# Optimization experiments

Hardware: AMD Instinct MI355X
Metric: run time of the kernel (lower is better)

The kernel has to match this reference:

```python
import jax, jax.numpy as jnp
import numpy as np

N_NODES = 100000
N_EDGES = 1600000
D = 128
NUM_CLASSES = 2
NEG_SLOPE = 0.01  # torch default leaky_relu slope


def setup_inputs() -> dict:
    key = jax.random.key(0)
    ks = jax.random.split(key, 12)
    s = 1.0 / np.sqrt(2 * D)
    return {
        "x": jax.random.normal(ks[0], (N_NODES, D), dtype=jnp.float32),
        "edge_src": jax.random.randint(ks[1], (N_EDGES,), 0, N_NODES, dtype=jnp.int32),
        "edge_dst": jax.random.randint(ks[2], (N_EDGES,), 0, N_NODES, dtype=jnp.int32),
        "edge_w1": jax.random.uniform(ks[3], (N_EDGES,), dtype=jnp.float32),
        "edge_w2": jax.random.uniform(ks[4], (N_EDGES,), dtype=jnp.float32),
        "W1": jax.random.normal(ks[5], (2 * D, D), dtype=jnp.float32) * s,
        "b1": jnp.zeros((D,), dtype=jnp.float32),
        "W2": jax.random.normal(ks[6], (2 * D, D), dtype=jnp.float32) * s,
        "b2": jnp.zeros((D,), dtype=jnp.float32),
        "Wl1": jax.random.normal(ks[7], (D, D), dtype=jnp.float32) * (1.0 / np.sqrt(D)),
        "bl1": jnp.zeros((D,), dtype=jnp.float32),
        "Wl2": jax.random.normal(ks[8], (D, NUM_CLASSES), dtype=jnp.float32) * (1.0 / np.sqrt(D)),
        "bl2": jnp.zeros((NUM_CLASSES,), dtype=jnp.float32),
    }


def _sage_conv(x, src, dst, ew, W, b, deg_inv):
    # weighted SpMM with reduce='mean': sum_e(w_e * x[src_e]) / rowcount(dst)
    msg = ew[:, None] * x[src]                                   # [E, D]
    agg = jax.ops.segment_sum(msg, dst, num_segments=N_NODES)    # [N, D]
    agg = agg * deg_inv[:, None]
    agg = jax.nn.leaky_relu(agg, NEG_SLOPE)
    h = jnp.concatenate([x, agg], axis=-1)                       # [N, 2D]
    return h @ W + b


def reference(x, edge_src, edge_dst, edge_w1, edge_w2,
              W1, b1, W2, b2, Wl1, bl1, Wl2, bl2):
    deg = jax.ops.segment_sum(jnp.ones((N_EDGES,), jnp.float32), edge_dst,
                              num_segments=N_NODES)
    deg_inv = jnp.where(deg > 0, 1.0 / jnp.maximum(deg, 1.0), 0.0)
    h = jax.nn.relu(_sage_conv(x, edge_src, edge_dst, edge_w1, W1, b1, deg_inv))
    h = jax.nn.relu(_sage_conv(h, edge_src, edge_dst, edge_w2, W2, b2, deg_inv))
    # train_status=False -> dropout is identity
    scores = jax.nn.relu(h @ Wl1 + bl1)
    scores = scores @ Wl2 + bl2                                  # [N, num_classes]
    return scores
```

## Files before the change

kernel.cpp:

```cpp
#include <hip/hip_runtime.h>
#include <hip/hip_fp16.h>

#define N_NODES 100000
#define N_EDGES 1600000
#define D 128

#define NBIN 196
#define NCHUNK 391
#define CHUNK_E 4096
#define SCAN_TOT (NBIN * NCHUNK)
#define SC_NB ((SCAN_TOT + 1023) / 1024)

#define WT_BLK 320
#define CVT_BLK 6250

typedef __attribute__((ext_vector_type(8))) _Float16 f16x8;
typedef __attribute__((ext_vector_type(4))) float f32x4;

__device__ __forceinline__ float h2f(ushort u) {
    __half_raw r; r.x = u;
    return __half2float(__half(r));
}
__device__ __forceinline__ ushort f2h(float f) {
    __half_raw r = __half_raw(__float2half(f));
    return r.x;
}


__global__ __launch_bounds__(256) void prep_kernel(const int* __restrict__ dst,
                                                   int* __restrict__ blockhist,
                                                   const float* __restrict__ W1,
                                                   const float* __restrict__ W2,
                                                   const float* __restrict__ Wl1,
                                                   ushort* __restrict__ W1t,
                                                   ushort* __restrict__ W2t,
                                                   ushort* __restrict__ Wl1t,
                                                   const float* __restrict__ x,
                                                   ushort* __restrict__ xf) {
    __shared__ int h[NBIN];
    int tid = threadIdx.x;
    int b = blockIdx.x;
    if (b < NCHUNK) {
        for (int i = tid; i < NBIN; i += 256) h[i] = 0;
        __syncthreads();
        int base = b * CHUNK_E;
#pragma unroll
        for (int j = 0; j < 16; ++j) {
            int i = base + j * 256 + tid;
            if (i < N_EDGES) atomicAdd(&h[dst[i] >> 9], 1);
        }
        __syncthreads();
        for (int i = tid; i < NBIN; i += 256)
            blockhist[i * NCHUNK + b] = h[i];
    } else if (b < NCHUNK + WT_BLK) {
        int i = (b - NCHUNK) * 256 + tid;
        const int DD2 = 2 * D * D;
        const float* src; ushort* dstp; int j;
        if (i < DD2)                  { src = W1;  dstp = W1t;  j = i; }
        else if (i < 2 * DD2)         { src = W2;  dstp = W2t;  j = i - DD2; }
        else                          { src = Wl1; dstp = Wl1t; j = i - 2 * DD2; }
        int k = j >> 7, n = j & 127;
        int addr = (((k >> 3) << 7) + n) * 8 + (k & 7);
        dstp[addr] = f2h(src[j]);
    } else {
        long i = ((long)(b - NCHUNK - WT_BLK) * 256 + tid) * 8;
        const float4 a = *reinterpret_cast<const float4*>(&x[i]);
        const float4 c = *reinterpret_cast<const float4*>(&x[i + 4]);
        ushort4 u0, u1;
        u0.x = f2h(a.x); u0.y = f2h(a.y); u0.z = f2h(a.z); u0.w = f2h(a.w);
        u1.x = f2h(c.x); u1.y = f2h(c.y); u1.z = f2h(c.z); u1.w = f2h(c.w);
        *reinterpret_cast<ushort4*>(&xf[i]) = u0;
        *reinterpret_cast<ushort4*>(&xf[i + 4]) = u1;
    }
}


__global__ __launch_bounds__(256) void scan_a(const int* __restrict__ bh,
                                              int* __restrict__ partials) {
    __shared__ int sums[256];
    int tid = threadIdx.x;
    int base = blockIdx.x * 1024 + tid * 4;
    int s = 0;
#pragma unroll
    for (int i = 0; i < 4; ++i) {
        int idx = base + i;
        if (idx < SCAN_TOT) s += bh[idx];
    }
    sums[tid] = s;
    __syncthreads();
#pragma unroll
    for (int off = 128; off > 0; off >>= 1) {
        if (tid < off) sums[tid] += sums[tid + off];
        __syncthreads();
    }
    if (tid == 0) partials[blockIdx.x] = sums[0];
}

__global__ __launch_bounds__(256) void scan_c(int* __restrict__ bh,
                                              const int* __restrict__ partials,
                                              int* __restrict__ row_ptr) {
    __shared__ int tsum[256];
    __shared__ int red[128];
    __shared__ int offs;
    int tid = threadIdx.x;

    if (tid < 128) {
        int v = (tid < blockIdx.x) ? partials[tid] : 0;
        red[tid] = v;
    }
    __syncthreads();
#pragma unroll
    for (int off = 64; off > 0; off >>= 1) {
        if (tid < off) red[tid] += red[tid + off];
        __syncthreads();
    }
    if (tid == 0) {
        offs = red[0];
        if (blockIdx.x == 0) row_ptr[N_NODES] = N_EDGES;
    }
    __syncthreads();

    int base = blockIdx.x * 1024 + tid * 4;
    int d[4];
#pragma unroll
    for (int i = 0; i < 4; ++i)
        d[i] = (base + i < SCAN_TOT) ? bh[base + i] : 0;
    int s = d[0] + d[1] + d[2] + d[3];
    tsum[tid] = s;
    __syncthreads();
    for (int off = 1; off < 256; off <<= 1) {
        int t = (tid >= off) ? tsum[tid - off] : 0;
        __syncthreads();
        tsum[tid] += t;
        __syncthreads();
    }
    int run = offs + tsum[tid] - s;
#pragma unroll
    for (int i = 0; i < 4; ++i) {
        int idx = base + i;
        if (idx < SCAN_TOT) {
            bh[idx] = run;
            run += d[i];
        }
    }
}

__global__ __launch_bounds__(256) void p1_scatter(const int* __restrict__ src,
                                                  const int* __restrict__ dst,
                                                  const float* __restrict__ w1,
                                                  const float* __restrict__ w2,
                                                  const int* __restrict__ bh,
                                                  uint2* __restrict__ part) {
    __shared__ int cur[NBIN];
    int tid = threadIdx.x;
    for (int b = tid; b < NBIN; b += 256) cur[b] = bh[b * NCHUNK + blockIdx.x];
    __syncthreads();
    int base = blockIdx.x * CHUNK_E;
#pragma unroll
    for (int j = 0; j < 16; ++j) {
        int i = base + j * 256 + tid;
        if (i < N_EDGES) {
            int d = dst[i];
            int pos = atomicAdd(&cur[d >> 9], 1);
            uint2 e;
            e.x = (unsigned)src[i] | ((unsigned)(d & 511) << 17);
            e.y = (unsigned)f2h(w1[i]) | ((unsigned)f2h(w2[i]) << 16);
            part[pos] = e;
        }
    }
}


__global__ __launch_bounds__(256) void p2_kernel(const int* __restrict__ bh,
                                                 const uint2* __restrict__ part,
                                                 int* __restrict__ row_ptr,
                                                 uint2* __restrict__ packed) {
    __shared__ int deg2[512];
    __shared__ int cur[512];
    __shared__ int sb[256];
    int tid = threadIdx.x;
    int bin = blockIdx.x;
    int base = bh[bin * NCHUNK];
    int endv = (bin == NBIN - 1) ? N_EDGES : bh[(bin + 1) * NCHUNK];
    int cnt = endv - base;
    deg2[tid] = 0; deg2[tid + 256] = 0;
    __syncthreads();
    for (int k = tid; k < cnt; k += 256)
        atomicAdd(&deg2[part[base + k].x >> 17], 1);
    __syncthreads();
    int s0 = deg2[2 * tid], s1 = deg2[2 * tid + 1];
    int ts = s0 + s1;
    sb[tid] = ts;
    __syncthreads();
    for (int off = 1; off < 256; off <<= 1) {
        int v = (tid >= off) ? sb[tid - off] : 0;
        __syncthreads();
        sb[tid] += v;
        __syncthreads();
    }
    int ex = sb[tid] - ts;
    cur[2 * tid] = ex;
    cur[2 * tid + 1] = ex + s0;
    int node0 = bin * 512 + 2 * tid;
    if (node0 < N_NODES)     row_ptr[node0]     = base + ex;
    if (node0 + 1 < N_NODES) row_ptr[node0 + 1] = base + ex + s0;
    __syncthreads();
    for (int k = tid; k < cnt; k += 256) {
        uint2 r = part[base + k];
        int local = r.x >> 17;
        float di = 1.0f / (float)deg2[local];
        int pos = base + atomicAdd(&cur[local], 1);
        uint2 e;
        e.x = r.x & 0x1FFFFu;
        e.y = (unsigned)f2h(h2f((ushort)(r.y & 0xFFFFu)) * di)
            | ((unsigned)f2h(h2f((ushort)(r.y >> 16)) * di) << 16);
        packed[pos] = e;
    }
}


template<int WIDX>
__global__ __launch_bounds__(256) void spmm_kernel(const ushort* __restrict__ xin,
                                                   const uint2* __restrict__ edges,
                                                   const int* __restrict__ row_ptr,
                                                   ushort* __restrict__ out) {
    int wid = threadIdx.x >> 6;
    int lane = threadIdx.x & 63;
    int par = lane >> 4;
    int dl = lane & 15;
    int n = blockIdx.x * 4 + wid;
    int beg = row_ptr[n], end = row_ptr[n + 1];
    float a[8] = {0.f, 0.f, 0.f, 0.f, 0.f, 0.f, 0.f, 0.f};

    const _Float16* xh = reinterpret_cast<const _Float16*>(xin);

    int i = beg;
    for (; i + 15 < end; i += 16) {
        const uint2 e0 = edges[i + par];
        const uint2 e1 = edges[i + 4 + par];
        const uint2 e2 = edges[i + 8 + par];
        const uint2 e3 = edges[i + 12 + par];
        float w0 = (float)__builtin_bit_cast(_Float16, (ushort)(WIDX ? (e0.y >> 16) : (e0.y & 0xFFFFu)));
        float w1 = (float)__builtin_bit_cast(_Float16, (ushort)(WIDX ? (e1.y >> 16) : (e1.y & 0xFFFFu)));
        float w2 = (float)__builtin_bit_cast(_Float16, (ushort)(WIDX ? (e2.y >> 16) : (e2.y & 0xFFFFu)));
        float w3 = (float)__builtin_bit_cast(_Float16, (ushort)(WIDX ? (e3.y >> 16) : (e3.y & 0xFFFFu)));
        const f16x8 v0 = *reinterpret_cast<const f16x8*>(&xh[(long)e0.x * D + dl * 8]);
        const f16x8 v1 = *reinterpret_cast<const f16x8*>(&xh[(long)e1.x * D + dl * 8]);
        const f16x8 v2 = *reinterpret_cast<const f16x8*>(&xh[(long)e2.x * D + dl * 8]);
        const f16x8 v3 = *reinterpret_cast<const f16x8*>(&xh[(long)e3.x * D + dl * 8]);
#pragma unroll
        for (int j = 0; j < 8; ++j)
            a[j] += (float)v0[j] * w0 + (float)v1[j] * w1
                  + (float)v2[j] * w2 + (float)v3[j] * w3;
    }
    for (; i + 7 < end; i += 8) {
        const uint2 e0 = edges[i + par];
        const uint2 e1 = edges[i + 4 + par];
        float w0 = (float)__builtin_bit_cast(_Float16, (ushort)(WIDX ? (e0.y >> 16) : (e0.y & 0xFFFFu)));
        float w1 = (float)__builtin_bit_cast(_Float16, (ushort)(WIDX ? (e1.y >> 16) : (e1.y & 0xFFFFu)));
        const f16x8 v0 = *reinterpret_cast<const f16x8*>(&xh[(long)e0.x * D + dl * 8]);
        const f16x8 v1 = *reinterpret_cast<const f16x8*>(&xh[(long)e1.x * D + dl * 8]);
#pragma unroll
        for (int j = 0; j < 8; ++j)
            a[j] += (float)v0[j] * w0 + (float)v1[j] * w1;
    }
    for (; i < end; i += 4) {
        int idx = i + par;
        bool act = idx < end;
        const uint2 e0 = edges[act ? idx : end - 1];
        float w0 = act ? (float)__builtin_bit_cast(_Float16, (ushort)(WIDX ? (e0.y >> 16) : (e0.y & 0xFFFFu))) : 0.f;
        const f16x8 v0 = *reinterpret_cast<const f16x8*>(&xh[(long)e0.x * D + dl * 8]);
#pragma unroll
        for (int j = 0; j < 8; ++j)
            a[j] += (float)v0[j] * w0;
    }

#pragma unroll
    for (int j = 0; j < 8; ++j) {
        a[j] += __shfl_xor(a[j], 16, 64);
        a[j] += __shfl_xor(a[j], 32, 64);
    }

    if (par == 0) {
        ushort4 r0, r1;
        float v;
        v = a[0]; v = v > 0.f ? v : 0.01f * v; r0.x = f2h(v);
        v = a[1]; v = v > 0.f ? v : 0.01f * v; r0.y = f2h(v);
        v = a[2]; v = v > 0.f ? v : 0.01f * v; r0.z = f2h(v);
        v = a[3]; v = v > 0.f ? v : 0.01f * v; r0.w = f2h(v);
        v = a[4]; v = v > 0.f ? v : 0.01f * v; r1.x = f2h(v);
        v = a[5]; v = v > 0.f ? v : 0.01f * v; r1.y = f2h(v);
        v = a[6]; v = v > 0.f ? v : 0.01f * v; r1.z = f2h(v);
        v = a[7]; v = v > 0.f ? v : 0.01f * v; r1.w = f2h(v);
        *reinterpret_cast<ushort4*>(&out[(long)n * D + dl * 8]) = r0;
        *reinterpret_cast<ushort4*>(&out[(long)n * D + dl * 8 + 4]) = r1;
    }
}


__global__ __launch_bounds__(256) void gemm_mfma_kernel(
        const ushort* __restrict__ in1,
        const ushort* __restrict__ in2,
        const ushort* __restrict__ Wt,
        const float* __restrict__ bias,
        ushort* __restrict__ outp) {
    int tid = threadIdx.x;
    int w = tid >> 6, l = tid & 63;
    int c = l & 15, kg = l >> 4;
    int base_m = blockIdx.x * 64 + w * 16;
    int r0 = base_m + c;  if (r0 >= N_NODES) r0 = N_NODES - 1;

    f32x4 acc[8];
#pragma unroll
    for (int ni = 0; ni < 8; ++ni) acc[ni] = (f32x4)0.f;

    for (int ks = 0; ks < 8; ++ks) {
        int kb = (ks & 3) * 32 + kg * 8;
        const ushort* src = (ks < 4) ? in1 : in2;
        f16x8 a0 = *reinterpret_cast<const f16x8*>(&src[(long)r0 * D + kb]);
        const ushort* wb = &Wt[(size_t)((ks * 4 + kg) * 128) * 8];
#pragma unroll
        for (int ni = 0; ni < 8; ++ni) {
            const f16x8 b = *reinterpret_cast<const f16x8*>(&wb[(ni * 16 + c) * 8]);
            acc[ni] = __builtin_amdgcn_mfma_f32_16x16x32_f16(a0, b, acc[ni], 0, 0, 0);
        }
    }

    float bv[8];
#pragma unroll
    for (int ni = 0; ni < 8; ++ni) bv[ni] = bias[ni * 16 + c];
    int rowb = base_m + kg * 4;
#pragma unroll
    for (int r = 0; r < 4; ++r) {
        int row = rowb + r;
        if (row < N_NODES) {
#pragma unroll
            for (int ni = 0; ni < 8; ++ni) {
                float v = acc[ni][r] + bv[ni];
                v = v > 0.f ? v : 0.f;
                outp[(long)row * D + ni * 16 + c] = f2h(v);
            }
        }
    }
}


#define LSTR 136

__global__ __launch_bounds__(256) void gemm2_cls_kernel(
        const ushort* __restrict__ in1,
        const ushort* __restrict__ in2,
        const ushort* __restrict__ W2t,
        const float* __restrict__ b2,
        const ushort* __restrict__ Wl1t,
        const float* __restrict__ bl1,
        const float* __restrict__ Wl2,
        const float* __restrict__ bl2,
        float* __restrict__ out) {
    __shared__ __align__(16) ushort lds_h2[4][16][LSTR];
    int tid = threadIdx.x;
    int w = tid >> 6, l = tid & 63;
    int c = l & 15, kg = l >> 4;
    int base_m = blockIdx.x * 64 + w * 16;
    int r0 = base_m + c;  if (r0 >= N_NODES) r0 = N_NODES - 1;

    f32x4 acc[8];
#pragma unroll
    for (int ni = 0; ni < 8; ++ni) acc[ni] = (f32x4)0.f;

    for (int ks = 0; ks < 8; ++ks) {
        int kb = (ks & 3) * 32 + kg * 8;
        const ushort* src = (ks < 4) ? in1 : in2;
        f16x8 a0 = *reinterpret_cast<const f16x8*>(&src[(long)r0 * D + kb]);
        const ushort* wb = &W2t[(size_t)((ks * 4 + kg) * 128) * 8];
#pragma unroll
        for (int ni = 0; ni < 8; ++ni) {
            const f16x8 b = *reinterpret_cast<const f16x8*>(&wb[(ni * 16 + c) * 8]);
            acc[ni] = __builtin_amdgcn_mfma_f32_16x16x32_f16(a0, b, acc[ni], 0, 0, 0);
        }
    }

    float bv[8];
#pragma unroll
    for (int ni = 0; ni < 8; ++ni) bv[ni] = b2[ni * 16 + c];
#pragma unroll
    for (int r = 0; r < 4; ++r) {
        int lrow = kg * 4 + r;
#pragma unroll
        for (int ni = 0; ni < 8; ++ni) {
            float v = acc[ni][r] + bv[ni];
            v = v > 0.f ? v : 0.f;
            lds_h2[w][lrow][ni * 16 + c] = f2h(v);
        }
    }
    __syncthreads();

    f32x4 bcc[8];
#pragma unroll
    for (int ni = 0; ni < 8; ++ni) bcc[ni] = (f32x4)0.f;

    for (int ks = 0; ks < 4; ++ks) {
        int kb = ks * 32 + kg * 8;
        f16x8 a0 = *reinterpret_cast<const f16x8*>(&lds_h2[w][c][kb]);
        const ushort* wb = &Wl1t[(size_t)((ks * 4 + kg) * 128) * 8];
#pragma unroll
        for (int ni = 0; ni < 8; ++ni) {
            const f16x8 b = *reinterpret_cast<const f16x8*>(&wb[(ni * 16 + c) * 8]);
            bcc[ni] = __builtin_amdgcn_mfma_f32_16x16x32_f16(a0, b, bcc[ni], 0, 0, 0);
        }
    }

    float b1v[8]; float2 w2v[8];
#pragma unroll
    for (int ni = 0; ni < 8; ++ni) {
        b1v[ni] = bl1[ni * 16 + c];
        w2v[ni] = *reinterpret_cast<const float2*>(&Wl2[(ni * 16 + c) * 2]);
    }
    float p0[4] = {0.f, 0.f, 0.f, 0.f};
    float p1[4] = {0.f, 0.f, 0.f, 0.f};
#pragma unroll
    for (int ni = 0; ni < 8; ++ni) {
#pragma unroll
        for (int r = 0; r < 4; ++r) {
            float t = bcc[ni][r] + b1v[ni];
            t = t > 0.f ? t : 0.f;
            p0[r] += t * w2v[ni].x;
            p1[r] += t * w2v[ni].y;
        }
    }
#pragma unroll
    for (int r = 0; r < 4; ++r) {
#pragma unroll
        for (int m = 1; m < 16; m <<= 1) {
            p0[r] += __shfl_xor(p0[r], m, 64);
            p1[r] += __shfl_xor(p1[r], m, 64);
        }
    }
    if (c < 2) {
        int rowb = base_m + kg * 4;
#pragma unroll
        for (int r = 0; r < 4; ++r) {
            int row = rowb + r;
            if (row < N_NODES)
                out[(long)row * 2 + c] = (c == 0 ? p0[r] : p1[r]) + bl2[c];
        }
    }
}


extern "C" void kernel_launch(void* const* d_in, const int* in_sizes, int n_in,
                              void* d_out, int out_size, void* d_ws, size_t ws_size,
                              hipStream_t stream) {
    const float* x   = (const float*)d_in[0];
    const int* esrc  = (const int*)d_in[1];
    const int* edst  = (const int*)d_in[2];
    const float* ew1 = (const float*)d_in[3];
    const float* ew2 = (const float*)d_in[4];
    const float* W1  = (const float*)d_in[5];
    const float* b1  = (const float*)d_in[6];
    const float* W2  = (const float*)d_in[7];
    const float* b2  = (const float*)d_in[8];
    const float* Wl1 = (const float*)d_in[9];
    const float* bl1 = (const float*)d_in[10];
    const float* Wl2 = (const float*)d_in[11];
    const float* bl2 = (const float*)d_in[12];
    float* out = (float*)d_out;

    char* p = (char*)d_ws;
    ushort* Af      = (ushort*)p;          p += (size_t)N_NODES * D * 2;
    ushort* h1f     = (ushort*)p;          p += (size_t)N_NODES * D * 2;
    ushort* xf      = (ushort*)p;          p += (size_t)N_NODES * D * 2;
    int* row_ptr    = (int*)p;             p += (size_t)(N_NODES + 16) * 4;
    int* blockhist  = (int*)p;             p += (size_t)SCAN_TOT * 4;
    int* partials   = (int*)p;             p += 128 * 4;
    uint2* part     = (uint2*)p;           p += (size_t)N_EDGES * 8;
    uint2* packed   = (uint2*)p;           p += (size_t)N_EDGES * 8;
    ushort* W1t     = (ushort*)p;          p += 2 * D * D * 2;
    ushort* W2t     = (ushort*)p;          p += 2 * D * D * 2;
    ushort* Wl1t    = (ushort*)p;          p += D * D * 2;

    prep_kernel<<<NCHUNK + WT_BLK + CVT_BLK, 256, 0, stream>>>(
        edst, blockhist, W1, W2, Wl1, W1t, W2t, Wl1t, x, xf);
    scan_a<<<SC_NB, 256, 0, stream>>>(blockhist, partials);
    scan_c<<<SC_NB, 256, 0, stream>>>(blockhist, partials, row_ptr);
    p1_scatter<<<NCHUNK, 256, 0, stream>>>(esrc, edst, ew1, ew2, blockhist, part);
    p2_kernel<<<NBIN, 256, 0, stream>>>(blockhist, part, row_ptr, packed);

    int ggrid = (N_NODES + 63) / 64;

    spmm_kernel<0><<<N_NODES / 4, 256, 0, stream>>>(xf, packed, row_ptr, Af);
    gemm_mfma_kernel<<<ggrid, 256, 0, stream>>>(xf, Af, W1t, b1, h1f);
    spmm_kernel<1><<<N_NODES / 4, 256, 0, stream>>>(h1f, packed, row_ptr, Af);
    gemm2_cls_kernel<<<ggrid, 256, 0, stream>>>(h1f, Af, W2t, b2, Wl1t, bl1, Wl2, bl2, out);
}
```

Measured before the change: 243.3 us.

## Stage GEMM weights in LDS with 512-thread blocks; vectorize scatter edge loads

Both dense GEMM kernels now copy the full transposed 256x128 fp16 weight matrix (64 KB) into shared memory and run 512-thread blocks covering 128 rows each, so B-fragments come from LDS instead of repeated global/L2 reads. The second GEMM reuses that LDS buffer for the h2 staging tile after a barrier. Separately, the partition scatter kernel loads dst/src/weights as 4-wide vectors per thread. The 64 KB LDS per block limits occupancy, and each block pays an upfront weight copy.

```diff
diff --git a/kernel.cpp b/kernel.cpp
--- a/kernel.cpp
+++ b/kernel.cpp
@@ -157,15 +157,40 @@
     __syncthreads();
     int base = blockIdx.x * CHUNK_E;
 #pragma unroll
-    for (int j = 0; j < 16; ++j) {
-        int i = base + j * 256 + tid;
-        if (i < N_EDGES) {
-            int d = dst[i];
-            int pos = atomicAdd(&cur[d >> 9], 1);
+    for (int j = 0; j < 4; ++j) {
+        int i0 = base + (j * 256 + tid) * 4;
+        if (i0 + 3 < N_EDGES) {
+            const int4 d4 = *reinterpret_cast<const int4*>(&dst[i0]);
+            const int4 s4 = *reinterpret_cast<const int4*>(&src[i0]);
+            const float4 a4 = *reinterpret_cast<const float4*>(&w1[i0]);
+            const float4 b4 = *reinterpret_cast<const float4*>(&w2[i0]);
             uint2 e;
-            e.x = (unsigned)src[i] | ((unsigned)(d & 511) << 17);
-            e.y = (unsigned)f2h(w1[i]) | ((unsigned)f2h(w2[i]) << 16);
+            int pos;
+            pos = atomicAdd(&cur[d4.x >> 9], 1);
+            e.x = (unsigned)s4.x | ((unsigned)(d4.x & 511) << 17);
+            e.y = (unsigned)f2h(a4.x) | ((unsigned)f2h(b4.x) << 16);
             part[pos] = e;
+            pos = atomicAdd(&cur[d4.y >> 9], 1);
+            e.x = (unsigned)s4.y | ((unsigned)(d4.y & 511) << 17);
+            e.y = (unsigned)f2h(a4.y) | ((unsigned)f2h(b4.y) << 16);
+            part[pos] = e;
+            pos = atomicAdd(&cur[d4.z >> 9], 1);
+            e.x = (unsigned)s4.z | ((unsigned)(d4.z & 511) << 17);
+            e.y = (unsigned)f2h(a4.z) | ((unsigned)f2h(b4.z) << 16);
+            part[pos] = e;
+            pos = atomicAdd(&cur[d4.w >> 9], 1);
+            e.x = (unsigned)s4.w | ((unsigned)(d4.w & 511) << 17);
+            e.y = (unsigned)f2h(a4.w) | ((unsigned)f2h(b4.w) << 16);
+            part[pos] = e;
+        } else {
+            for (int i = i0; i < N_EDGES; ++i) {
+                int d = dst[i];
+                int pos = atomicAdd(&cur[d >> 9], 1);
+                uint2 e;
+                e.x = (unsigned)src[i] | ((unsigned)(d & 511) << 17);
+                e.y = (unsigned)f2h(w1[i]) | ((unsigned)f2h(w2[i]) << 16);
+                part[pos] = e;
+            }
         }
     }
 }
@@ -298,16 +323,27 @@
 }
 
 
-__global__ __launch_bounds__(256) void gemm_mfma_kernel(
+#define WSH (2 * D * D)
+
+__global__ __launch_bounds__(512) void gemm_mfma_kernel(
         const ushort* __restrict__ in1,
         const ushort* __restrict__ in2,
         const ushort* __restrict__ Wt,
         const float* __restrict__ bias,
         ushort* __restrict__ outp) {
-    int tid = threadIdx.x;
+    __shared__ __align__(16) ushort lds_w[WSH];
+    int tid = threadIdx.x;
+#pragma unroll
+    for (int it = 0; it < 8; ++it) {
+        int idx = it * 512 + tid;
+        *reinterpret_cast<f16x8*>(&lds_w[idx * 8]) =
+            *reinterpret_cast<const f16x8*>(&Wt[idx * 8]);
+    }
+    __syncthreads();
+
     int w = tid >> 6, l = tid & 63;
     int c = l & 15, kg = l >> 4;
-    int base_m = blockIdx.x * 64 + w * 16;
+    int base_m = blockIdx.x * 128 + w * 16;
     int r0 = base_m + c;  if (r0 >= N_NODES) r0 = N_NODES - 1;
 
     f32x4 acc[8];
@@ -318,7 +354,7 @@
         int kb = (ks & 3) * 32 + kg * 8;
         const ushort* src = (ks < 4) ? in1 : in2;
         f16x8 a0 = *reinterpret_cast<const f16x8*>(&src[(long)r0 * D + kb]);
-        const ushort* wb = &Wt[(size_t)((ks * 4 + kg) * 128) * 8];
+        const ushort* wb = &lds_w[(size_t)((ks * 4 + kg) * 128) * 8];
 #pragma unroll
         for (int ni = 0; ni < 8; ++ni) {
             const f16x8 b = *reinterpret_cast<const f16x8*>(&wb[(ni * 16 + c) * 8]);
@@ -347,7 +383,7 @@
 
 #define LSTR 136
 
-__global__ __launch_bounds__(256) void gemm2_cls_kernel(
+__global__ __launch_bounds__(512) void gemm2_cls_kernel(
         const ushort* __restrict__ in1,
         const ushort* __restrict__ in2,
         const ushort* __restrict__ W2t,
@@ -357,11 +393,19 @@
         const float* __restrict__ Wl2,
         const float* __restrict__ bl2,
         float* __restrict__ out) {
-    __shared__ __align__(16) ushort lds_h2[4][16][LSTR];
-    int tid = threadIdx.x;
+    __shared__ __align__(16) ushort lds_w[WSH];
+    int tid = threadIdx.x;
+#pragma unroll
+    for (int it = 0; it < 8; ++it) {
+        int idx = it * 512 + tid;
+        *reinterpret_cast<f16x8*>(&lds_w[idx * 8]) =
+            *reinterpret_cast<const f16x8*>(&W2t[idx * 8]);
+    }
+    __syncthreads();
+
     int w = tid >> 6, l = tid & 63;
     int c = l & 15, kg = l >> 4;
-    int base_m = blockIdx.x * 64 + w * 16;
+    int base_m = blockIdx.x * 128 + w * 16;
     int r0 = base_m + c;  if (r0 >= N_NODES) r0 = N_NODES - 1;
 
     f32x4 acc[8];
@@ -372,7 +416,7 @@
         int kb = (ks & 3) * 32 + kg * 8;
         const ushort* src = (ks < 4) ? in1 : in2;
         f16x8 a0 = *reinterpret_cast<const f16x8*>(&src[(long)r0 * D + kb]);
-        const ushort* wb = &W2t[(size_t)((ks * 4 + kg) * 128) * 8];
+        const ushort* wb = &lds_w[(size_t)((ks * 4 + kg) * 128) * 8];
 #pragma unroll
         for (int ni = 0; ni < 8; ++ni) {
             const f16x8 b = *reinterpret_cast<const f16x8*>(&wb[(ni * 16 + c) * 8]);
@@ -383,6 +427,9 @@
     float bv[8];
 #pragma unroll
     for (int ni = 0; ni < 8; ++ni) bv[ni] = b2[ni * 16 + c];
+
+    __syncthreads();
+    ushort* h2 = &lds_w[w * 16 * LSTR];
 #pragma unroll
     for (int r = 0; r < 4; ++r) {
         int lrow = kg * 4 + r;
@@ -390,7 +437,7 @@
         for (int ni = 0; ni < 8; ++ni) {
             float v = acc[ni][r] + bv[ni];
             v = v > 0.f ? v : 0.f;
-            lds_h2[w][lrow][ni * 16 + c] = f2h(v);
+            h2[lrow * LSTR + ni * 16 + c] = f2h(v);
         }
     }
     __syncthreads();
@@ -401,7 +448,7 @@
 
     for (int ks = 0; ks < 4; ++ks) {
         int kb = ks * 32 + kg * 8;
-        f16x8 a0 = *reinterpret_cast<const f16x8*>(&lds_h2[w][c][kb]);
+        f16x8 a0 = *reinterpret_cast<const f16x8*>(&h2[c * LSTR + kb]);
         const ushort* wb = &Wl1t[(size_t)((ks * 4 + kg) * 128) * 8];
 #pragma unroll
         for (int ni = 0; ni < 8; ++ni) {
@@ -486,10 +533,10 @@
     p1_scatter<<<NCHUNK, 256, 0, stream>>>(esrc, edst, ew1, ew2, blockhist, part);
     p2_kernel<<<NBIN, 256, 0, stream>>>(blockhist, part, row_ptr, packed);
 
-    int ggrid = (N_NODES + 63) / 64;
+    int ggrid = (N_NODES + 127) / 128;
 
     spmm_kernel<0><<<N_NODES / 4, 256, 0, stream>>>(xf, packed, row_ptr, Af);
-    gemm_mfma_kernel<<<ggrid, 256, 0, stream>>>(xf, Af, W1t, b1, h1f);
+    gemm_mfma_kernel<<<ggrid, 512, 0, stream>>>(xf, Af, W1t, b1, h1f);
     spmm_kernel<1><<<N_NODES / 4, 256, 0, stream>>>(h1f, packed, row_ptr, Af);
-    gemm2_cls_kernel<<<ggrid, 256, 0, stream>>>(h1f, Af, W2t, b2, Wl1t, bl1, Wl2, bl2, out);
-}
+    gemm2_cls_kernel<<<ggrid, 512, 0, stream>>>(h1f, Af, W2t, b2, Wl1t, bl1, Wl2, bl2, out);
+}
```

New measurement: 222.7 us (median of 2 runs). 8.4% less time.
